# Kernel tuning notes

Hardware: AMD Instinct MI355X
Metric: run time of the kernel (lower is better)

## Reference

```python
import jax, jax.numpy as jnp
import numpy as np

B, S, D, H, E = 4, 2048, 1024, 4096, 8
THRESHOLD = 0.5


def setup_inputs() -> dict:
    key = jax.random.key(0)
    ks = jax.random.split(key, 7)
    s_in = 1.0 / np.sqrt(D)
    s_h = 1.0 / np.sqrt(H)
    return {
        "x": jax.random.normal(ks[0], (B, S, D), dtype=jnp.float32),
        "Wg": jax.random.uniform(ks[1], (D, E), jnp.float32, -s_in, s_in),
        "bg": jax.random.uniform(ks[2], (E,), jnp.float32, -s_in, s_in),
        "W1": jax.random.uniform(ks[3], (E, D, H), jnp.float32, -s_in, s_in),
        "b1": jax.random.uniform(ks[4], (E, H), jnp.float32, -s_in, s_in),
        "W2": jax.random.uniform(ks[5], (E, H, D), jnp.float32, -s_h, s_h),
        "b2": jax.random.uniform(ks[6], (E, D), jnp.float32, -s_h, s_h),
    }


def reference(x, Wg, bg, W1, b1, W2, b2):
    b, s, d = x.shape
    x_flat = x.reshape(-1, d)                       # [T, D], T = B*S
    # Top-any gating: sigmoid logits, threshold mask, weights = probs * mask
    probs = jax.nn.sigmoid(x_flat @ Wg + bg)        # [T, E]
    mask = (probs > THRESHOLD).astype(x_flat.dtype)
    weights = probs * mask                          # [T, E]
    # Dense per-expert MLP over all tokens (faithful to the torch loop)
    h = jax.nn.relu(jnp.einsum('td,edh->eth', x_flat, W1) + b1[:, None, :])  # [E, T, H]
    expert_out = jnp.einsum('eth,ehd->etd', h, W2) + b2[:, None, :]          # [E, T, D]
    combined = jnp.einsum('te,etd->td', weights, expert_out)                 # [T, D]
    return combined.reshape(b, s, d)
```

## Files before the change

### kernel.cpp

```cpp
#include <hip/hip_runtime.h>
#include <hip/hip_bf16.h>

#define T_TOK 8192
#define D_DIM 1024
#define H_DIM 4096
#define E_NUM 8
#define IDXST 8448
#define CAPBLK 18
#define CAPROWS (CAPBLK * 256)

typedef short bf16x8 __attribute__((ext_vector_type(8)));
typedef float f32x4 __attribute__((ext_vector_type(4)));

__device__ __forceinline__ unsigned short f2bf(float f) {
    union { float f; unsigned int u; } v; v.f = f;
    unsigned int u = v.u;
    u = u + 0x7FFFu + ((u >> 16) & 1u);
    return (unsigned short)(u >> 16);
}

__device__ __forceinline__ void gload_lds16(const void* g, void* l) {
    __builtin_amdgcn_global_load_lds(
        (const __attribute__((address_space(1))) unsigned int*)g,
        (__attribute__((address_space(3))) unsigned int*)l,
        16, 0, 0);
}

#define SBAR() { __builtin_amdgcn_sched_barrier(0); __builtin_amdgcn_s_barrier(); __builtin_amdgcn_sched_barrier(0); }
#define LGKM0() { asm volatile("s_waitcnt lgkmcnt(0)" ::: "memory"); __builtin_amdgcn_sched_barrier(0); }
#define VMC4() { asm volatile("s_waitcnt vmcnt(4)" ::: "memory"); __builtin_amdgcn_sched_barrier(0); }
#define VMC0() { asm volatile("s_waitcnt vmcnt(0)" ::: "memory"); __builtin_amdgcn_sched_barrier(0); }

__device__ __forceinline__ void swz_bmbn(int lin, int nbm, int nbn, int& bm, int& bn) {
    const int nwg = nbm * nbn;
    int wgid = ((nwg & 7) == 0) ? ((lin & 7) * (nwg >> 3) + (lin >> 3)) : lin;
    if ((nbm & 7) == 0 && (nbn & 3) == 0) {
        const int per = nbn << 3;
        int stripe = wgid / per;
        int l = wgid - stripe * per;
        int g = l >> 5, r = l & 31;
        bm = stripe * 8 + (r >> 2);
        bn = g * 4 + (r & 3);
    } else {
        bm = wgid / nbn;
        bn = wgid - bm * nbn;
    }
}

__device__ __forceinline__ int swz_rt(int lin, int n) {
    int q = n >> 3, r = n & 7;
    int xcd = lin & 7, pos = lin >> 3;
    int base = (xcd < r) ? xcd * (q + 1) : r * (q + 1) + (xcd - r) * q;
    return base + pos;
}

template<int NBN>
__device__ __forceinline__ bool merged_map(const int* __restrict__ cntp,
                                           int& e, int& bm, int& bn, int& cnt_e) {
    int nbs[E_NUM], tot = 0;
    #pragma unroll
    for (int i = 0; i < E_NUM; ++i) {
        int c = cntp[i];
        int nbm = (c + 255) >> 8;
        if (nbm > CAPBLK) nbm = CAPBLK;
        nbs[i] = nbm * NBN;
        tot += nbs[i];
    }
    if ((int)blockIdx.x >= tot) return false;
    const int wg = swz_rt(blockIdx.x, tot);
    int acc = 0, loc = 0;
    e = 0;
    #pragma unroll
    for (int i = 0; i < E_NUM; ++i) {
        if (wg >= acc && wg < acc + nbs[i]) { e = i; loc = wg - acc; }
        acc += nbs[i];
    }
    bm = loc / NBN;
    bn = loc - bm * NBN;
    cnt_e = cntp[e];
    return true;
}

__global__ void gate_cvt_kernel(const float* __restrict__ x, const float* __restrict__ Wg,
                                const float* __restrict__ bg, float* __restrict__ wout,
                                unsigned short* __restrict__ xb) {
    int wv = (int)((blockIdx.x * blockDim.x + threadIdx.x) >> 6);
    int lane = threadIdx.x & 63;
    if (wv >= T_TOK) return;
    const float* xr = x + (size_t)wv * D_DIM;
    unsigned short* xo = xb + (size_t)wv * D_DIM;
    double acc[E_NUM] = {0, 0, 0, 0, 0, 0, 0, 0};
    for (int i = 0; i < D_DIM / 64; ++i) {
        int d = i * 64 + lane;
        float xf = xr[d];
        xo[d] = f2bf(xf);
        double xv = (double)xf;
        const float* wr = Wg + (size_t)d * E_NUM;
        #pragma unroll
        for (int e = 0; e < E_NUM; ++e) acc[e] += xv * (double)wr[e];
    }
    #pragma unroll
    for (int e = 0; e < E_NUM; ++e) {
        double v = acc[e];
        for (int s = 32; s; s >>= 1) v += __shfl_down(v, s, 64);
        acc[e] = v;
    }
    if (lane == 0) {
        #pragma unroll
        for (int e = 0; e < E_NUM; ++e) {
            double z = acc[e] + (double)bg[e];
            float p = (float)(1.0 / (1.0 + exp(-z)));
            wout[(size_t)wv * E_NUM + e] = (p > 0.5f) ? p : 0.0f;
        }
    }
}

__global__ void compact_kernel(const float* __restrict__ wgt, int* __restrict__ idx,
                               float* __restrict__ wc, int* __restrict__ cnt) {
    const int e = blockIdx.x;
    const int tid = threadIdx.x;
    const int lane = tid & 63, wv = tid >> 6;
    int* idxe = idx + e * IDXST;
    float* wce = wc + e * IDXST;
    __shared__ int wtot[4];
    __shared__ int sbase;
    if (tid == 0) sbase = 0;
    __syncthreads();
    for (int t0 = 0; t0 < T_TOK; t0 += 256) {
        int t = t0 + tid;
        float w = wgt[(size_t)t * E_NUM + e];
        int act = (w > 0.0f) ? 1 : 0;
        unsigned long long mask = __ballot(act);
        int wpos = __popcll(mask & ((1ull << lane) - 1ull));
        if (lane == 0) wtot[wv] = __popcll(mask);
        __syncthreads();
        int off = sbase;
        for (int i = 0; i < wv; ++i) off += wtot[i];
        if (act) { idxe[off + wpos] = t; wce[off + wpos] = w; }
        __syncthreads();
        if (tid == 0) sbase += wtot[0] + wtot[1] + wtot[2] + wtot[3];
        __syncthreads();
    }
    int total = sbase;
    int padded = ((total + 255) / 256) * 256;
    for (int i = total + tid; i < padded; i += 256) { idxe[i] = 0; wce[i] = 0.0f; }
    if (tid == 0) cnt[e] = total;
}

__global__ void transpose_cvt(const float* __restrict__ in, unsigned short* __restrict__ out,
                              int R, int C) {
    __shared__ unsigned short tile[64][65];
    int e = blockIdx.z;
    const float* src = in + (size_t)e * R * C;
    unsigned short* dst = out + (size_t)e * R * C;
    int c0 = blockIdx.x * 64, r0 = blockIdx.y * 64;
    int t = threadIdx.x;
    int cc = (t & 15) * 4;
    int rr = t >> 4;
    #pragma unroll
    for (int p = 0; p < 4; ++p) {
        int r = rr + p * 16;
        float4 v = *(const float4*)(src + (size_t)(r0 + r) * C + c0 + cc);
        tile[cc + 0][r] = f2bf(v.x);
        tile[cc + 1][r] = f2bf(v.y);
        tile[cc + 2][r] = f2bf(v.z);
        tile[cc + 3][r] = f2bf(v.w);
    }
    __syncthreads();
    int rr4 = (t & 15) * 4;
    int cw = t >> 4;
    #pragma unroll
    for (int p = 0; p < 4; ++p) {
        int c = cw + p * 16;
        ushort4 o;
        o.x = tile[c][rr4 + 0];
        o.y = tile[c][rr4 + 1];
        o.z = tile[c][rr4 + 2];
        o.w = tile[c][rr4 + 3];
        *(ushort4*)(dst + (size_t)(c0 + c) * R + r0 + rr4) = o;
    }
}

__global__ void zero_kernel(float4* __restrict__ p, size_t n4) {
    size_t i = (size_t)blockIdx.x * blockDim.x + threadIdx.x;
    size_t st = (size_t)gridDim.x * blockDim.x;
    for (; i < n4; i += st) p[i] = (float4){0.f, 0.f, 0.f, 0.f};
}

__global__ void sentinel_kernel(float* out, size_t n) {
    size_t i = (size_t)blockIdx.x * blockDim.x + threadIdx.x;
    size_t st = (size_t)gridDim.x * blockDim.x;
    for (; i < n; i += st) out[i] = 12345.0f;
}

__global__ __launch_bounds__(512, 2) void gemm1c(
    const unsigned short* __restrict__ Xb,
    const unsigned short* __restrict__ W1T,
    unsigned short* __restrict__ Hc,
    const float* __restrict__ b1,
    const int* __restrict__ idxb,
    const float* __restrict__ wcb,
    const int* __restrict__ cntp)
{
    __shared__ __align__(16) unsigned short lA[2][16384];
    __shared__ __align__(16) unsigned short lB[2][16384];

    int e, bm, bn, cnt;
    if (!merged_map<H_DIM / 256>(cntp, e, bm, bn, cnt)) return;

    const int* idx = idxb + e * IDXST;
    const float* wc = wcb + e * IDXST;
    const unsigned short* Bmat = W1T + (size_t)e * H_DIM * D_DIM;
    const float* b1e = b1 + (size_t)e * H_DIM;
    unsigned short* HcE = Hc + (size_t)e * CAPROWS * H_DIM;

    const int tid = threadIdx.x;
    const int lane = tid & 63, wid = tid >> 6;
    const int wr = wid >> 2;
    const int wcn = wid & 3;
    const int fr = lane & 15, fq = lane >> 4;

    const int srow = tid >> 3;
    const int scol = (((tid & 7) ^ (srow & 7)) << 3);

    const unsigned short* Asrc[4];
    #pragma unroll
    for (int h = 0; h < 4; ++h)
        Asrc[h] = Xb + (size_t)idx[bm * 256 + h * 64 + srow] * D_DIM + scol;
    const unsigned short* Bb = Bmat + (size_t)(bn * 256 + srow) * D_DIM + scol;

    const int s0 = ((0 << 2) | fq) ^ (fr & 7);
    const int s1 = ((1 << 2) | fq) ^ (fr & 7);

    f32x4 acc[8][4];
    #pragma unroll
    for (int m = 0; m < 8; ++m)
        #pragma unroll
        for (int n = 0; n < 4; ++n)
            acc[m][n] = (f32x4){0.f, 0.f, 0.f, 0.f};

    bf16x8 a[4][2], b[4][2];

    auto stageA = [&](int bf, int hf, int kt) {
        gload_lds16(Asrc[hf * 2]     + kt * 64, &lA[bf][hf * 8192 + tid * 8]);
        gload_lds16(Asrc[hf * 2 + 1] + kt * 64, &lA[bf][hf * 8192 + 4096 + tid * 8]);
    };
    auto stageB = [&](int bf, int hf, int kt) {
        const unsigned short* s = Bb + (size_t)(hf * 128) * D_DIM + kt * 64;
        gload_lds16(s,                      &lB[bf][hf * 8192 + tid * 8]);
        gload_lds16(s + (size_t)64 * D_DIM, &lB[bf][hf * 8192 + 4096 + tid * 8]);
    };

    stageB(0, 0, 0);
    stageA(0, 0, 0);
    stageA(0, 1, 0);
    stageB(0, 1, 0);
    stageB(1, 0, 1);
    stageA(1, 0, 1);
    VMC4();
    SBAR();

    int cur = 0;
    const int NT = D_DIM / 64;
    for (int t = 0; t < NT; ++t) {
        const int nxt = cur ^ 1;
        #pragma unroll
        for (int mm = 0; mm < 4; ++mm) {
            const int r = wr * 128 + mm * 16 + fr;
            a[mm][0] = *(const bf16x8*)&lA[cur][r * 64 + s0 * 8];
            a[mm][1] = *(const bf16x8*)&lA[cur][r * 64 + s1 * 8];
        }
        #pragma unroll
        for (int n = 0; n < 2; ++n) {
            const int r = wcn * 64 + n * 16 + fr;
            b[n][0] = *(const bf16x8*)&lB[cur][r * 64 + s0 * 8];
            b[n][1] = *(const bf16x8*)&lB[cur][r * 64 + s1 * 8];
        }
        if (t + 1 < NT) stageA(nxt, 1, t + 1);
        SBAR(); LGKM0();
        __builtin_amdgcn_s_setprio(1);
        #pragma unroll
        for (int kk = 0; kk < 2; ++kk)
            #pragma unroll
            for (int mm = 0; mm < 4; ++mm) {
                acc[mm][0] = __builtin_amdgcn_mfma_f32_16x16x32_bf16(a[mm][kk], b[0][kk], acc[mm][0], 0, 0, 0);
                acc[mm][1] = __builtin_amdgcn_mfma_f32_16x16x32_bf16(a[mm][kk], b[1][kk], acc[mm][1], 0, 0, 0);
            }
        __builtin_amdgcn_s_setprio(0);
        SBAR();
        #pragma unroll
        for (int n = 2; n < 4; ++n) {
            const int r = wcn * 64 + n * 16 + fr;
            b[n][0] = *(const bf16x8*)&lB[cur][r * 64 + s0 * 8];
            b[n][1] = *(const bf16x8*)&lB[cur][r * 64 + s1 * 8];
        }
        if (t + 1 < NT) stageB(nxt, 1, t + 1);
        SBAR(); LGKM0();
        __builtin_amdgcn_s_setprio(1);
        #pragma unroll
        for (int kk = 0; kk < 2; ++kk)
            #pragma unroll
            for (int mm = 0; mm < 4; ++mm) {
                acc[mm][2] = __builtin_amdgcn_mfma_f32_16x16x32_bf16(a[mm][kk], b[2][kk], acc[mm][2], 0, 0, 0);
                acc[mm][3] = __builtin_amdgcn_mfma_f32_16x16x32_bf16(a[mm][kk], b[3][kk], acc[mm][3], 0, 0, 0);
            }
        __builtin_amdgcn_s_setprio(0);
        SBAR();
        #pragma unroll
        for (int mm = 0; mm < 4; ++mm) {
            const int r = wr * 128 + (mm + 4) * 16 + fr;
            a[mm][0] = *(const bf16x8*)&lA[cur][r * 64 + s0 * 8];
            a[mm][1] = *(const bf16x8*)&lA[cur][r * 64 + s1 * 8];
        }
        if (t + 2 < NT) stageB(cur, 0, t + 2);
        SBAR(); LGKM0();
        __builtin_amdgcn_s_setprio(1);
        #pragma unroll
        for (int kk = 0; kk < 2; ++kk)
            #pragma unroll
            for (int mm = 0; mm < 4; ++mm) {
                acc[mm + 4][0] = __builtin_amdgcn_mfma_f32_16x16x32_bf16(a[mm][kk], b[0][kk], acc[mm + 4][0], 0, 0, 0);
                acc[mm + 4][1] = __builtin_amdgcn_mfma_f32_16x16x32_bf16(a[mm][kk], b[1][kk], acc[mm + 4][1], 0, 0, 0);
            }
        __builtin_amdgcn_s_setprio(0);
        SBAR();
        if (t + 2 < NT) stageA(cur, 0, t + 2);
        if (t < NT - 2) { VMC4(); } else { VMC0(); }
        SBAR(); LGKM0();
        __builtin_amdgcn_s_setprio(1);
        #pragma unroll
        for (int kk = 0; kk < 2; ++kk)
            #pragma unroll
            for (int mm = 0; mm < 4; ++mm) {
                acc[mm + 4][2] = __builtin_amdgcn_mfma_f32_16x16x32_bf16(a[mm][kk], b[2][kk], acc[mm + 4][2], 0, 0, 0);
                acc[mm + 4][3] = __builtin_amdgcn_mfma_f32_16x16x32_bf16(a[mm][kk], b[3][kk], acc[mm + 4][3], 0, 0, 0);
            }
        __builtin_amdgcn_s_setprio(0);
        SBAR();
        cur = nxt;
    }

    #pragma unroll
    for (int m = 0; m < 8; ++m) {
        const int rbase = bm * 256 + wr * 128 + m * 16 + fq * 4;
        #pragma unroll
        for (int n = 0; n < 4; ++n) {
            const int cn = bn * 256 + wcn * 64 + n * 16 + fr;
            const float bb = b1e[cn];
            #pragma unroll
            for (int j = 0; j < 4; ++j) {
                const int r = rbase + j;
                const float w = wc[r];
                float v = fmaxf(acc[m][n][j] + bb, 0.0f) * w;
                HcE[(size_t)r * H_DIM + cn] = f2bf(v);
            }
        }
    }
}

__global__ __launch_bounds__(512, 2) void gemm2c(
    const unsigned short* __restrict__ Hc,
    const unsigned short* __restrict__ W2T,
    float* __restrict__ out,
    const float* __restrict__ b2,
    const int* __restrict__ idxb,
    const float* __restrict__ wcb,
    const int* __restrict__ cntp)
{
    __shared__ __align__(16) unsigned short lA[2][16384];
    __shared__ __align__(16) unsigned short lB[2][16384];

    int e, bm, bn, cnt;
    if (!merged_map<D_DIM / 256>(cntp, e, bm, bn, cnt)) return;

    const int* idx = idxb + e * IDXST;
    const float* wc = wcb + e * IDXST;
    const unsigned short* A = Hc + (size_t)e * CAPROWS * H_DIM;
    const unsigned short* Bmat = W2T + (size_t)e * D_DIM * H_DIM;
    const float* b2e = b2 + (size_t)e * D_DIM;

    const int tid = threadIdx.x;
    const int lane = tid & 63, wid = tid >> 6;
    const int wr = wid >> 2;
    const int wcn = wid & 3;
    const int fr = lane & 15, fq = lane >> 4;

    const int srow = tid >> 3;
    const int scol = (((tid & 7) ^ (srow & 7)) << 3);
    const unsigned short* Ab = A + (size_t)(bm * 256 + srow) * H_DIM + scol;
    const unsigned short* Bb = Bmat + (size_t)(bn * 256 + srow) * H_DIM + scol;

    const int s0 = ((0 << 2) | fq) ^ (fr & 7);
    const int s1 = ((1 << 2) | fq) ^ (fr & 7);

    f32x4 acc[8][4];
    #pragma unroll
    for (int m = 0; m < 8; ++m)
        #pragma unroll
        for (int n = 0; n < 4; ++n)
            acc[m][n] = (f32x4){0.f, 0.f, 0.f, 0.f};

    bf16x8 a[4][2], b[4][2];

    auto stageA = [&](int bf, int hf, int kt) {
        const unsigned short* s = Ab + (size_t)(hf * 128) * H_DIM + kt * 64;
        gload_lds16(s,                      &lA[bf][hf * 8192 + tid * 8]);
        gload_lds16(s + (size_t)64 * H_DIM, &lA[bf][hf * 8192 + 4096 + tid * 8]);
    };
    auto stageB = [&](int bf, int hf, int kt) {
        const unsigned short* s = Bb + (size_t)(hf * 128) * H_DIM + kt * 64;
        gload_lds16(s,                      &lB[bf][hf * 8192 + tid * 8]);
        gload_lds16(s + (size_t)64 * H_DIM, &lB[bf][hf * 8192 + 4096 + tid * 8]);
    };

    stageB(0, 0, 0);
    stageA(0, 0, 0);
    stageA(0, 1, 0);
    stageB(0, 1, 0);
    stageB(1, 0, 1);
    stageA(1, 0, 1);
    VMC4();
    SBAR();

    int cur = 0;
    const int NT = H_DIM / 64;
    for (int t = 0; t < NT; ++t) {
        const int nxt = cur ^ 1;
        #pragma unroll
        for (int mm = 0; mm < 4; ++mm) {
            const int r = wr * 128 + mm * 16 + fr;
            a[mm][0] = *(const bf16x8*)&lA[cur][r * 64 + s0 * 8];
            a[mm][1] = *(const bf16x8*)&lA[cur][r * 64 + s1 * 8];
        }
        #pragma unroll
        for (int n = 0; n < 2; ++n) {
            const int r = wcn * 64 + n * 16 + fr;
            b[n][0] = *(const bf16x8*)&lB[cur][r * 64 + s0 * 8];
            b[n][1] = *(const bf16x8*)&lB[cur][r * 64 + s1 * 8];
        }
        if (t + 1 < NT) stageA(nxt, 1, t + 1);
        SBAR(); LGKM0();
        __builtin_amdgcn_s_setprio(1);
        #pragma unroll
        for (int kk = 0; kk < 2; ++kk)
            #pragma unroll
            for (int mm = 0; mm < 4; ++mm) {
                acc[mm][0] = __builtin_amdgcn_mfma_f32_16x16x32_bf16(a[mm][kk], b[0][kk], acc[mm][0], 0, 0, 0);
                acc[mm][1] = __builtin_amdgcn_mfma_f32_16x16x32_bf16(a[mm][kk], b[1][kk], acc[mm][1], 0, 0, 0);
            }
        __builtin_amdgcn_s_setprio(0);
        SBAR();
        #pragma unroll
        for (int n = 2; n < 4; ++n) {
            const int r = wcn * 64 + n * 16 + fr;
            b[n][0] = *(const bf16x8*)&lB[cur][r * 64 + s0 * 8];
            b[n][1] = *(const bf16x8*)&lB[cur][r * 64 + s1 * 8];
        }
        if (t + 1 < NT) stageB(nxt, 1, t + 1);
        SBAR(); LGKM0();
        __builtin_amdgcn_s_setprio(1);
        #pragma unroll
        for (int kk = 0; kk < 2; ++kk)
            #pragma unroll
            for (int mm = 0; mm < 4; ++mm) {
                acc[mm][2] = __builtin_amdgcn_mfma_f32_16x16x32_bf16(a[mm][kk], b[2][kk], acc[mm][2], 0, 0, 0);
                acc[mm][3] = __builtin_amdgcn_mfma_f32_16x16x32_bf16(a[mm][kk], b[3][kk], acc[mm][3], 0, 0, 0);
            }
        __builtin_amdgcn_s_setprio(0);
        SBAR();
        #pragma unroll
        for (int mm = 0; mm < 4; ++mm) {
            const int r = wr * 128 + (mm + 4) * 16 + fr;
            a[mm][0] = *(const bf16x8*)&lA[cur][r * 64 + s0 * 8];
            a[mm][1] = *(const bf16x8*)&lA[cur][r * 64 + s1 * 8];
        }
        if (t + 2 < NT) stageB(cur, 0, t + 2);
        SBAR(); LGKM0();
        __builtin_amdgcn_s_setprio(1);
        #pragma unroll
        for (int kk = 0; kk < 2; ++kk)
            #pragma unroll
            for (int mm = 0; mm < 4; ++mm) {
                acc[mm + 4][0] = __builtin_amdgcn_mfma_f32_16x16x32_bf16(a[mm][kk], b[0][kk], acc[mm + 4][0], 0, 0, 0);
                acc[mm + 4][1] = __builtin_amdgcn_mfma_f32_16x16x32_bf16(a[mm][kk], b[1][kk], acc[mm + 4][1], 0, 0, 0);
            }
        __builtin_amdgcn_s_setprio(0);
        SBAR();
        if (t + 2 < NT) stageA(cur, 0, t + 2);
        if (t < NT - 2) { VMC4(); } else { VMC0(); }
        SBAR(); LGKM0();
        __builtin_amdgcn_s_setprio(1);
        #pragma unroll
        for (int kk = 0; kk < 2; ++kk)
            #pragma unroll
            for (int mm = 0; mm < 4; ++mm) {
                acc[mm + 4][2] = __builtin_amdgcn_mfma_f32_16x16x32_bf16(a[mm][kk], b[2][kk], acc[mm + 4][2], 0, 0, 0);
                acc[mm + 4][3] = __builtin_amdgcn_mfma_f32_16x16x32_bf16(a[mm][kk], b[3][kk], acc[mm + 4][3], 0, 0, 0);
            }
        __builtin_amdgcn_s_setprio(0);
        SBAR();
        cur = nxt;
    }

    #pragma unroll
    for (int m = 0; m < 8; ++m) {
        const int rbase = bm * 256 + wr * 128 + m * 16 + fq * 4;
        #pragma unroll
        for (int n = 0; n < 4; ++n) {
            const int cn = bn * 256 + wcn * 64 + n * 16 + fr;
            const float bb = b2e[cn];
            #pragma unroll
            for (int j = 0; j < 4; ++j) {
                const int row = rbase + j;
                if (row < cnt) {
                    const int tok = idx[row];
                    atomicAdd(&out[(size_t)tok * D_DIM + cn], acc[m][n][j] + wc[row] * bb);
                }
            }
        }
    }
}

__global__ __launch_bounds__(512, 2) void gemm1_8ph(
    const unsigned short* __restrict__ A,
    const unsigned short* __restrict__ W1T,
    unsigned short* __restrict__ Hc,
    const float* __restrict__ b1,
    const float* __restrict__ wgt,
    int t0, int e, int nbm)
{
    __shared__ __align__(16) unsigned short lA[2][16384];
    __shared__ __align__(16) unsigned short lB[2][16384];
    const int nbn = H_DIM / 256;
    int bm, bn;
    swz_bmbn(blockIdx.x, nbm, nbn, bm, bn);
    const int tid = threadIdx.x;
    const int lane = tid & 63, wid = tid >> 6;
    const int wr = wid >> 2;
    const int wcn = wid & 3;
    const int fr = lane & 15, fq = lane >> 4;
    const int srow = tid >> 3;
    const int scol = (((tid & 7) ^ (srow & 7)) << 3);
    const unsigned short* Ab = A + (size_t)(bm * 256 + srow) * D_DIM + scol;
    const unsigned short* Bb = W1T + (size_t)e * H_DIM * D_DIM
                             + (size_t)(bn * 256 + srow) * D_DIM + scol;
    const int s0 = ((0 << 2) | fq) ^ (fr & 7);
    const int s1 = ((1 << 2) | fq) ^ (fr & 7);
    f32x4 acc[8][4];
    #pragma unroll
    for (int m = 0; m < 8; ++m)
        #pragma unroll
        for (int n = 0; n < 4; ++n)
            acc[m][n] = (f32x4){0.f, 0.f, 0.f, 0.f};
    bf16x8 a[4][2], b[4][2];
    auto stageA = [&](int bf, int hf, int kt) {
        const unsigned short* s = Ab + (size_t)(hf * 128) * D_DIM + kt * 64;
        gload_lds16(s,                      &lA[bf][hf * 8192 + tid * 8]);
        gload_lds16(s + (size_t)64 * D_DIM, &lA[bf][hf * 8192 + 4096 + tid * 8]);
    };
    auto stageB = [&](int bf, int hf, int kt) {
        const unsigned short* s = Bb + (size_t)(hf * 128) * D_DIM + kt * 64;
        gload_lds16(s,                      &lB[bf][hf * 8192 + tid * 8]);
        gload_lds16(s + (size_t)64 * D_DIM, &lB[bf][hf * 8192 + 4096 + tid * 8]);
    };
    stageB(0, 0, 0); stageA(0, 0, 0); stageA(0, 1, 0); stageB(0, 1, 0);
    stageB(1, 0, 1); stageA(1, 0, 1);
    VMC4();
    SBAR();
    int cur = 0;
    for (int t = 0; t < 16; ++t) {
        const int nxt = cur ^ 1;
        #pragma unroll
        for (int mm = 0; mm < 4; ++mm) {
            const int r = wr * 128 + mm * 16 + fr;
            a[mm][0] = *(const bf16x8*)&lA[cur][r * 64 + s0 * 8];
            a[mm][1] = *(const bf16x8*)&lA[cur][r * 64 + s1 * 8];
        }
        #pragma unroll
        for (int n = 0; n < 2; ++n) {
            const int r = wcn * 64 + n * 16 + fr;
            b[n][0] = *(const bf16x8*)&lB[cur][r * 64 + s0 * 8];
            b[n][1] = *(const bf16x8*)&lB[cur][r * 64 + s1 * 8];
        }
        if (t + 1 < 16) stageA(nxt, 1, t + 1);
        SBAR(); LGKM0();
        __builtin_amdgcn_s_setprio(1);
        #pragma unroll
        for (int kk = 0; kk < 2; ++kk)
            #pragma unroll
            for (int mm = 0; mm < 4; ++mm) {
                acc[mm][0] = __builtin_amdgcn_mfma_f32_16x16x32_bf16(a[mm][kk], b[0][kk], acc[mm][0], 0, 0, 0);
                acc[mm][1] = __builtin_amdgcn_mfma_f32_16x16x32_bf16(a[mm][kk], b[1][kk], acc[mm][1], 0, 0, 0);
            }
        __builtin_amdgcn_s_setprio(0);
        SBAR();
        #pragma unroll
        for (int n = 2; n < 4; ++n) {
            const int r = wcn * 64 + n * 16 + fr;
            b[n][0] = *(const bf16x8*)&lB[cur][r * 64 + s0 * 8];
            b[n][1] = *(const bf16x8*)&lB[cur][r * 64 + s1 * 8];
        }
        if (t + 1 < 16) stageB(nxt, 1, t + 1);
        SBAR(); LGKM0();
        __builtin_amdgcn_s_setprio(1);
        #pragma unroll
        for (int kk = 0; kk < 2; ++kk)
            #pragma unroll
            for (int mm = 0; mm < 4; ++mm) {
                acc[mm][2] = __builtin_amdgcn_mfma_f32_16x16x32_bf16(a[mm][kk], b[2][kk], acc[mm][2], 0, 0, 0);
                acc[mm][3] = __builtin_amdgcn_mfma_f32_16x16x32_bf16(a[mm][kk], b[3][kk], acc[mm][3], 0, 0, 0);
            }
        __builtin_amdgcn_s_setprio(0);
        SBAR();
        #pragma unroll
        for (int mm = 0; mm < 4; ++mm) {
            const int r = wr * 128 + (mm + 4) * 16 + fr;
            a[mm][0] = *(const bf16x8*)&lA[cur][r * 64 + s0 * 8];
            a[mm][1] = *(const bf16x8*)&lA[cur][r * 64 + s1 * 8];
        }
        if (t + 2 < 16) stageB(cur, 0, t + 2);
        SBAR(); LGKM0();
        __builtin_amdgcn_s_setprio(1);
        #pragma unroll
        for (int kk = 0; kk < 2; ++kk)
            #pragma unroll
            for (int mm = 0; mm < 4; ++mm) {
                acc[mm + 4][0] = __builtin_amdgcn_mfma_f32_16x16x32_bf16(a[mm][kk], b[0][kk], acc[mm + 4][0], 0, 0, 0);
                acc[mm + 4][1] = __builtin_amdgcn_mfma_f32_16x16x32_bf16(a[mm][kk], b[1][kk], acc[mm + 4][1], 0, 0, 0);
            }
        __builtin_amdgcn_s_setprio(0);
        SBAR();
        if (t + 2 < 16) stageA(cur, 0, t + 2);
        if (t < 14) { VMC4(); } else { VMC0(); }
        SBAR(); LGKM0();
        __builtin_amdgcn_s_setprio(1);
        #pragma unroll
        for (int kk = 0; kk < 2; ++kk)
            #pragma unroll
            for (int mm = 0; mm < 4; ++mm) {
                acc[mm + 4][2] = __builtin_amdgcn_mfma_f32_16x16x32_bf16(a[mm][kk], b[2][kk], acc[mm + 4][2], 0, 0, 0);
                acc[mm + 4][3] = __builtin_amdgcn_mfma_f32_16x16x32_bf16(a[mm][kk], b[3][kk], acc[mm + 4][3], 0, 0, 0);
            }
        __builtin_amdgcn_s_setprio(0);
        SBAR();
        cur = nxt;
    }
    #pragma unroll
    for (int m = 0; m < 8; ++m) {
        const int rbase = bm * 256 + wr * 128 + m * 16 + fq * 4;
        #pragma unroll
        for (int n = 0; n < 4; ++n) {
            const int cn = bn * 256 + wcn * 64 + n * 16 + fr;
            const float bb = b1[(size_t)e * H_DIM + cn];
            #pragma unroll
            for (int j = 0; j < 4; ++j) {
                const int r = rbase + j;
                const float w = wgt[(size_t)(t0 + r) * E_NUM + e];
                float v = fmaxf(acc[m][n][j] + bb, 0.0f) * w;
                Hc[(size_t)r * H_DIM + cn] = f2bf(v);
            }
        }
    }
}

template<int MODE>
__global__ __launch_bounds__(512, 2) void gemm2_8ph(
    const unsigned short* __restrict__ A,
    const unsigned short* __restrict__ B,
    float* __restrict__ out,
    const float* __restrict__ bias,
    const float* __restrict__ wts,
    int t0, int e, int nbm)
{
    __shared__ __align__(16) unsigned short lA[3][16384];
    __shared__ __align__(16) unsigned short lB[3][8192];
    const int nbn = D_DIM / 128;
    int bm, bn;
    swz_bmbn(blockIdx.x, nbm, nbn, bm, bn);
    const int tid = threadIdx.x;
    const int lane = tid & 63, wid = tid >> 6;
    const int wr = wid >> 1;
    const int wcn = wid & 1;
    const int fr = lane & 15, fq = lane >> 4;
    const int srow = tid >> 3;
    const int scol = (((tid & 7) ^ (srow & 7)) << 3);
    const unsigned short* Ab = A + (size_t)(bm * 256 + srow) * H_DIM + scol;
    const unsigned short* Bb = B + (size_t)(bn * 128 + srow) * H_DIM + scol;
    const int s0 = ((0 << 2) | fq) ^ (fr & 7);
    const int s1 = ((1 << 2) | fq) ^ (fr & 7);
    f32x4 acc[4][4];
    #pragma unroll
    for (int m = 0; m < 4; ++m)
        #pragma unroll
        for (int n = 0; n < 4; ++n)
            acc[m][n] = (f32x4){0.f, 0.f, 0.f, 0.f};
    bf16x8 a[4][2], b[4][2];
    auto stageA = [&](int bf, int hf, int kt) {
        const unsigned short* s = Ab + (size_t)(hf * 128) * H_DIM + kt * 64;
        gload_lds16(s,                      &lA[bf][hf * 8192 + tid * 8]);
        gload_lds16(s + (size_t)64 * H_DIM, &lA[bf][hf * 8192 + 4096 + tid * 8]);
    };
    auto stageB = [&](int bf, int kt) {
        const unsigned short* s = Bb + kt * 64;
        gload_lds16(s,                      &lB[bf][tid * 8]);
        gload_lds16(s + (size_t)64 * H_DIM, &lB[bf][4096 + tid * 8]);
    };
    stageA(0, 0, 0); stageA(0, 1, 0); stageB(0, 0);
    stageA(1, 0, 1); stageA(1, 1, 1); stageB(1, 1);
    asm volatile("s_waitcnt vmcnt(6)" ::: "memory"); __builtin_amdgcn_sched_barrier(0);
    SBAR();
    int bt = 0, bs = 2;
    const int NT = H_DIM / 64;
    for (int t = 0; t < NT; ++t) {
        #pragma unroll
        for (int mm = 0; mm < 4; ++mm) {
            const int r = wr * 64 + mm * 16 + fr;
            a[mm][0] = *(const bf16x8*)&lA[bt][r * 64 + s0 * 8];
            a[mm][1] = *(const bf16x8*)&lA[bt][r * 64 + s1 * 8];
        }
        #pragma unroll
        for (int n = 0; n < 2; ++n) {
            const int r = wcn * 64 + n * 16 + fr;
            b[n][0] = *(const bf16x8*)&lB[bt][r * 64 + s0 * 8];
            b[n][1] = *(const bf16x8*)&lB[bt][r * 64 + s1 * 8];
        }
        if (t + 2 < NT) { stageA(bs, 1, t + 2); stageB(bs, t + 2); }
        SBAR(); LGKM0();
        __builtin_amdgcn_s_setprio(1);
        #pragma unroll
        for (int kk = 0; kk < 2; ++kk)
            #pragma unroll
            for (int mm = 0; mm < 4; ++mm) {
                acc[mm][0] = __builtin_amdgcn_mfma_f32_16x16x32_bf16(a[mm][kk], b[0][kk], acc[mm][0], 0, 0, 0);
                acc[mm][1] = __builtin_amdgcn_mfma_f32_16x16x32_bf16(a[mm][kk], b[1][kk], acc[mm][1], 0, 0, 0);
            }
        __builtin_amdgcn_s_setprio(0);
        SBAR();
        #pragma unroll
        for (int n = 2; n < 4; ++n) {
            const int r = wcn * 64 + n * 16 + fr;
            b[n][0] = *(const bf16x8*)&lB[bt][r * 64 + s0 * 8];
            b[n][1] = *(const bf16x8*)&lB[bt][r * 64 + s1 * 8];
        }
        if (t + 2 < NT) { stageA(bs, 0, t + 2); asm volatile("s_waitcnt vmcnt(6)" ::: "memory"); __builtin_amdgcn_sched_barrier(0); } else { VMC0(); }
        SBAR(); LGKM0();
        __builtin_amdgcn_s_setprio(1);
        #pragma unroll
        for (int kk = 0; kk < 2; ++kk)
            #pragma unroll
            for (int mm = 0; mm < 4; ++mm) {
                acc[mm][2] = __builtin_amdgcn_mfma_f32_16x16x32_bf16(a[mm][kk], b[2][kk], acc[mm][2], 0, 0, 0);
                acc[mm][3] = __builtin_amdgcn_mfma_f32_16x16x32_bf16(a[mm][kk], b[3][kk], acc[mm][3], 0, 0, 0);
            }
        __builtin_amdgcn_s_setprio(0);
        SBAR();
        bt = (bt == 2) ? 0 : bt + 1;
        bs = (bs == 2) ? 0 : bs + 1;
    }
    #pragma unroll
    for (int m = 0; m < 4; ++m) {
        const int rbase = bm * 256 + wr * 64 + m * 16 + fq * 4;
        #pragma unroll
        for (int n = 0; n < 4; ++n) {
            const int cn = bn * 128 + wcn * 64 + n * 16 + fr;
            const float bb = bias[cn];
            #pragma unroll
            for (int j = 0; j < 4; ++j) {
                const int row = t0 + rbase + j;
                const float w = wts[(size_t)row * E_NUM + e];
                const float v = acc[m][n][j] + w * bb;
                float* p = out + (size_t)row * D_DIM + cn;
                if (MODE == 1) *p = v;
                else *p += v;
            }
        }
    }
}

extern "C" void kernel_launch(void* const* d_in, const int* in_sizes, int n_in,
                              void* d_out, int out_size, void* d_ws, size_t ws_size,
                              hipStream_t stream) {
    const float* x  = (const float*)d_in[0];
    const float* Wg = (const float*)d_in[1];
    const float* bg = (const float*)d_in[2];
    const float* W1 = (const float*)d_in[3];
    const float* b1 = (const float*)d_in[4];
    const float* W2 = (const float*)d_in[5];
    const float* b2 = (const float*)d_in[6];
    float* out = (float*)d_out;
    char* ws = (char*)d_ws;

    const size_t off_w   = 0;
    const size_t off_idx = 262144;
    const size_t off_wcc = 557056;
    const size_t off_cnt = 851968;
    const size_t off_x   = 1048576;
    const size_t off_w1  = off_x + (size_t)T_TOK * D_DIM * 2;
    const size_t off_w2  = off_w1 + (size_t)E_NUM * D_DIM * H_DIM * 2;
    const size_t off_h   = off_w2 + (size_t)E_NUM * D_DIM * H_DIM * 2;
    const size_t cap_h   = (size_t)E_NUM * CAPROWS * H_DIM * 2;
    const size_t min_h   = (size_t)256 * H_DIM * 2;

    if (ws_size < off_h + min_h) {
        sentinel_kernel<<<2048, 256, 0, stream>>>(out, (size_t)T_TOK * D_DIM);
        return;
    }

    float* wgt = (float*)(ws + off_w);
    int* idxb  = (int*)(ws + off_idx);
    float* wcb = (float*)(ws + off_wcc);
    int* cntb  = (int*)(ws + off_cnt);
    unsigned short* Xb  = (unsigned short*)(ws + off_x);
    unsigned short* W1T = (unsigned short*)(ws + off_w1);
    unsigned short* W2T = (unsigned short*)(ws + off_w2);
    unsigned short* Hc  = (unsigned short*)(ws + off_h);

    gate_cvt_kernel<<<T_TOK / 4, 256, 0, stream>>>(x, Wg, bg, wgt, Xb);
    transpose_cvt<<<dim3(H_DIM / 64, D_DIM / 64, E_NUM), 256, 0, stream>>>(W1, W1T, D_DIM, H_DIM);
    transpose_cvt<<<dim3(D_DIM / 64, H_DIM / 64, E_NUM), 256, 0, stream>>>(W2, W2T, H_DIM, D_DIM);

    if (ws_size >= off_h + cap_h) {
        compact_kernel<<<E_NUM, 256, 0, stream>>>(wgt, idxb, wcb, cntb);
        zero_kernel<<<2048, 256, 0, stream>>>((float4*)out, (size_t)T_TOK * D_DIM / 4);
        const int g1 = E_NUM * CAPBLK * (H_DIM / 256);
        const int g2 = E_NUM * CAPBLK * (D_DIM / 256);
        gemm1c<<<g1, 512, 0, stream>>>(Xb, W1T, Hc, b1, idxb, wcb, cntb);
        gemm2c<<<g2, 512, 0, stream>>>(Hc, W2T, out, b2, idxb, wcb, cntb);
    } else {
        size_t avail = ws_size - off_h;
        size_t tc = avail / ((size_t)H_DIM * 2);
        tc = (tc / 256) * 256;
        if (tc > T_TOK) tc = T_TOK;
        const int TC = (int)tc;
        for (int t0 = 0; t0 < T_TOK; t0 += TC) {
            int cs = (T_TOK - t0 < TC) ? (T_TOK - t0) : TC;
            const int nbm = cs / 256;
            for (int e = 0; e < E_NUM; ++e) {
                gemm1_8ph<<<nbm * (H_DIM / 256), 512, 0, stream>>>(
                    Xb + (size_t)t0 * D_DIM, W1T, Hc, b1, wgt, t0, e, nbm);
                if (e == 0)
                    gemm2_8ph<1><<<nbm * (D_DIM / 128), 512, 0, stream>>>(
                        Hc, W2T + (size_t)e * D_DIM * H_DIM, out,
                        b2 + (size_t)e * D_DIM, wgt, t0, e, nbm);
                else
                    gemm2_8ph<2><<<nbm * (D_DIM / 128), 512, 0, stream>>>(
                        Hc, W2T + (size_t)e * D_DIM * H_DIM, out,
                        b2 + (size_t)e * D_DIM, wgt, t0, e, nbm);
            }
        }
    }
}
```

Baseline: 1.044 ms.

## Triple-buffer A tiles in gemm2c to deepen A prefetch distance

The second expert GEMM now keeps three LDS buffers for the A (hidden activations) tile and two for B. A is prefetched two k-steps ahead and B one step ahead, replacing the old mixed-staging schedule that reused the current buffer. The goal is to hide more global-load latency for A. LDS use rises to 160KB, so launch bounds drop to one block per CU, cutting occupancy.

```diff
diff --git a/kernel.cpp b/kernel.cpp
--- a/kernel.cpp
+++ b/kernel.cpp
@@ -358,7 +358,7 @@
     }
 }
 
-__global__ __launch_bounds__(512, 2) void gemm2c(
+__global__ __launch_bounds__(512, 1) void gemm2c(
     const unsigned short* __restrict__ Hc,
     const unsigned short* __restrict__ W2T,
     float* __restrict__ out,
@@ -367,7 +367,7 @@
     const float* __restrict__ wcb,
     const int* __restrict__ cntp)
 {
-    __shared__ __align__(16) unsigned short lA[2][16384];
+    __shared__ __align__(16) unsigned short lA[3][16384];
     __shared__ __align__(16) unsigned short lB[2][16384];
 
     int e, bm, bn, cnt;
@@ -413,32 +413,30 @@
         gload_lds16(s + (size_t)64 * H_DIM, &lB[bf][hf * 8192 + 4096 + tid * 8]);
     };
 
-    stageB(0, 0, 0);
-    stageA(0, 0, 0);
-    stageA(0, 1, 0);
-    stageB(0, 1, 0);
-    stageB(1, 0, 1);
-    stageA(1, 0, 1);
+    stageA(0, 0, 0); stageA(0, 1, 0);
+    stageB(0, 0, 0); stageB(0, 1, 0);
+    stageA(1, 0, 1); stageA(1, 1, 1);
     VMC4();
     SBAR();
 
-    int cur = 0;
     const int NT = H_DIM / 64;
+    int at = 0, bt = 0;
     for (int t = 0; t < NT; ++t) {
-        const int nxt = cur ^ 1;
+        const int an2 = (at + 2 >= 3) ? at - 1 : at + 2;
+        const int bn1 = bt ^ 1;
         #pragma unroll
         for (int mm = 0; mm < 4; ++mm) {
             const int r = wr * 128 + mm * 16 + fr;
-            a[mm][0] = *(const bf16x8*)&lA[cur][r * 64 + s0 * 8];
-            a[mm][1] = *(const bf16x8*)&lA[cur][r * 64 + s1 * 8];
+            a[mm][0] = *(const bf16x8*)&lA[at][r * 64 + s0 * 8];
+            a[mm][1] = *(const bf16x8*)&lA[at][r * 64 + s1 * 8];
         }
         #pragma unroll
         for (int n = 0; n < 2; ++n) {
             const int r = wcn * 64 + n * 16 + fr;
-            b[n][0] = *(const bf16x8*)&lB[cur][r * 64 + s0 * 8];
-            b[n][1] = *(const bf16x8*)&lB[cur][r * 64 + s1 * 8];
-        }
-        if (t + 1 < NT) stageA(nxt, 1, t + 1);
+            b[n][0] = *(const bf16x8*)&lB[bt][r * 64 + s0 * 8];
+            b[n][1] = *(const bf16x8*)&lB[bt][r * 64 + s1 * 8];
+        }
+        if (t + 1 < NT) stageB(bn1, 0, t + 1);
         SBAR(); LGKM0();
         __builtin_amdgcn_s_setprio(1);
         #pragma unroll
@@ -453,10 +451,10 @@
         #pragma unroll
         for (int n = 2; n < 4; ++n) {
             const int r = wcn * 64 + n * 16 + fr;
-            b[n][0] = *(const bf16x8*)&lB[cur][r * 64 + s0 * 8];
-            b[n][1] = *(const bf16x8*)&lB[cur][r * 64 + s1 * 8];
-        }
-        if (t + 1 < NT) stageB(nxt, 1, t + 1);
+            b[n][0] = *(const bf16x8*)&lB[bt][r * 64 + s0 * 8];
+            b[n][1] = *(const bf16x8*)&lB[bt][r * 64 + s1 * 8];
+        }
+        if (t + 1 < NT) stageB(bn1, 1, t + 1);
         SBAR(); LGKM0();
         __builtin_amdgcn_s_setprio(1);
         #pragma unroll
@@ -471,10 +469,10 @@
         #pragma unroll
         for (int mm = 0; mm < 4; ++mm) {
             const int r = wr * 128 + (mm + 4) * 16 + fr;
-            a[mm][0] = *(const bf16x8*)&lA[cur][r * 64 + s0 * 8];
-            a[mm][1] = *(const bf16x8*)&lA[cur][r * 64 + s1 * 8];
-        }
-        if (t + 2 < NT) stageB(cur, 0, t + 2);
+            a[mm][0] = *(const bf16x8*)&lA[at][r * 64 + s0 * 8];
+            a[mm][1] = *(const bf16x8*)&lA[at][r * 64 + s1 * 8];
+        }
+        if (t + 2 < NT) stageA(an2, 0, t + 2);
         SBAR(); LGKM0();
         __builtin_amdgcn_s_setprio(1);
         #pragma unroll
@@ -486,7 +484,7 @@
             }
         __builtin_amdgcn_s_setprio(0);
         SBAR();
-        if (t + 2 < NT) stageA(cur, 0, t + 2);
+        if (t + 2 < NT) stageA(an2, 1, t + 2);
         if (t < NT - 2) { VMC4(); } else { VMC0(); }
         SBAR(); LGKM0();
         __builtin_amdgcn_s_setprio(1);
@@ -499,7 +497,8 @@
             }
         __builtin_amdgcn_s_setprio(0);
         SBAR();
-        cur = nxt;
+        at = (at == 2) ? 0 : at + 1;
+        bt = bn1;
     }
 
     #pragma unroll
```

After: 991.9 us. 5.0% less time.
